# Kernel tuning notes

Measured on AMD Instinct MI355X. Metric: run time of the kernel, lower is better.

Reference implementation:

```python
import jax, jax.numpy as jnp
import numpy as np

B, IB, H, W = 32, 103, 256, 256
P, RB, DIM, DEPTH = 16, 8, 192, 3
KS, KP, TOPK, NC = 24, 24, 2, 9
FFH = 2 * DIM  # max(64, int(dim*2)) = 384
TAU = 0.07 + 1e-08


def ln(x, w, b, eps=1e-5):
    m = x.mean(-1, keepdims=True)
    v = ((x - m) ** 2).mean(-1, keepdims=True)
    return (x - m) / jnp.sqrt(v + eps) * w + b


def setup_inputs() -> dict:
    key = jax.random.key(0)
    keys = iter(jax.random.split(key, 40))
    nrm = lambda shape, s=0.02: jax.random.normal(next(keys), shape, jnp.float32) * s
    return {
        "x": jax.random.normal(next(keys), (B, IB, H, W), jnp.float32),
        "band_w": nrm((RB, IB), 0.05), "band_b": jnp.zeros((RB,), jnp.float32),
        "dw_w": nrm((RB, P, P), 0.05), "pw_w": nrm((DIM, RB), 0.1),
        "pe_ln_w": jnp.ones((DIM,), jnp.float32), "pe_ln_b": jnp.zeros((DIM,), jnp.float32),
        "spec_proto": nrm((KS, RB)), "spat_proto": nrm((KP, DIM)),
        "r1_w": nrm((DIM, 128), 0.05), "r1_b": jnp.zeros((128,), jnp.float32),
        "r2_w": nrm((128, KS + KP), 0.05), "r2_b": jnp.zeros((KS + KP,), jnp.float32),
        "key_w": nrm((RB + DIM, DIM), 0.05),
        "pos_bias": jnp.zeros((1, 1, DIM), jnp.float32),
        "blk_ln_w": jnp.ones((DEPTH, DIM), jnp.float32), "blk_ln_b": jnp.zeros((DEPTH, DIM), jnp.float32),
        "blk_q_w": nrm((DEPTH, DIM, DIM), 0.05), "blk_v_w": nrm((DEPTH, DIM, DIM), 0.05),
        "blk_f1_w": nrm((DEPTH, DIM, FFH), 0.05), "blk_f1_b": jnp.zeros((DEPTH, FFH), jnp.float32),
        "blk_f2_w": nrm((DEPTH, FFH, DIM), 0.05), "blk_f2_b": jnp.zeros((DEPTH, DIM), jnp.float32),
        "blk_g1": jnp.full((DEPTH, DIM), 0.01, jnp.float32), "blk_g2": jnp.full((DEPTH, DIM), 0.01, jnp.float32),
        "fin_ln_w": jnp.ones((DIM,), jnp.float32), "fin_ln_b": jnp.zeros((DIM,), jnp.float32),
        "head_w": nrm((DIM, NC), 0.01), "head_b": jnp.zeros((NC,), jnp.float32),
    }


def _forward(x, band_w, band_b, dw_w, pw_w, pe_ln_w, pe_ln_b, spec_proto, spat_proto,
             r1_w, r1_b, r2_w, r2_b, key_w, pos_bias,
             blk_ln_w, blk_ln_b, blk_q_w, blk_v_w, blk_f1_w, blk_f1_b, blk_f2_w, blk_f2_b,
             blk_g1, blk_g2, fin_ln_w, fin_ln_b, head_w, head_b):
    # 1x1 band reduction conv: (B,103,H,W) -> (B,8,H,W)
    x_red = jnp.einsum('bchw,oc->bohw', x, band_w) + band_b[None, :, None, None]
    Bn, C, Hh, Ww = x_red.shape
    hp, wp = Hh // P, Ww // P
    # depthwise conv, kernel==stride==P -> non-overlapping patches
    patches = x_red.reshape(Bn, C, hp, P, wp, P)
    dw = jnp.einsum('bcipjq,cpq->bcij', patches, dw_w)        # (B,RB,hp,wp)
    pw = jnp.einsum('bcij,dc->bdij', dw, pw_w)                # (B,DIM,hp,wp)
    tok = pw.reshape(Bn, DIM, hp * wp).transpose(0, 2, 1)     # (B,N,DIM)
    tok = ln(tok, pe_ln_w, pe_ln_b)
    # router -> topk -> softmax gate -> gather prototypes -> weighted sum
    h = jax.nn.gelu(tok @ r1_w + r1_b, approximate=False)
    rlogits = h @ r2_w + r2_b                                 # (B,N,KS+KP)
    s_vals, s_idx = jax.lax.top_k(rlogits[..., :KS], TOPK)
    p_vals, p_idx = jax.lax.top_k(rlogits[..., KS:], TOPK)
    w_s = jax.nn.softmax(s_vals / TAU, axis=-1)               # (B,N,TOPK)
    w_p = jax.nn.softmax(p_vals / TAU, axis=-1)
    spec_mixed = (spec_proto[s_idx] * w_s[..., None]).sum(2)  # (B,N,RB)
    spat_mixed = (spat_proto[p_idx] * w_p[..., None]).sum(2)  # (B,N,DIM)
    keys_t = jnp.concatenate([spec_mixed, spat_mixed], -1) @ key_w + pos_bias  # (B,N,DIM)
    # linear-attention blocks
    xb = tok
    for i in range(DEPTH):
        xn = ln(xb, blk_ln_w[i], blk_ln_b[i])
        q = xn @ blk_q_w[i]
        v = xn @ blk_v_w[i]
        q_s = jax.nn.softmax(q, axis=-1)
        KV = jnp.einsum('bnc,bnd->bcd', keys_t, v)            # (B,C,C)
        out = jnp.einsum('bnc,bcd->bnd', q_s, KV)             # (B,N,C)
        xb = xb + out * blk_g1[i]
        xn2 = ln(xb, blk_ln_w[i], blk_ln_b[i])
        ff = jax.nn.gelu(xn2 @ blk_f1_w[i] + blk_f1_b[i], approximate=False) @ blk_f2_w[i] + blk_f2_b[i]
        xb = xb + ff * blk_g2[i]
    feat = ln(xb.mean(1), fin_ln_w, fin_ln_b)                 # (B,DIM)
    return feat @ head_w + head_b                             # (B,NC)


def reference(x, band_w, band_b, dw_w, pw_w, pe_ln_w, pe_ln_b, spec_proto, spat_proto,
              r1_w, r1_b, r2_w, r2_b, key_w, pos_bias,
              blk_ln_w, blk_ln_b, blk_q_w, blk_v_w, blk_f1_w, blk_f1_b, blk_f2_w, blk_f2_b,
              blk_g1, blk_g2, fin_ln_w, fin_ln_b, head_w, head_b):
    return _forward(x, band_w, band_b, dw_w, pw_w, pe_ln_w, pe_ln_b, spec_proto, spat_proto,
                    r1_w, r1_b, r2_w, r2_b, key_w, pos_bias,
                    blk_ln_w, blk_ln_b, blk_q_w, blk_v_w, blk_f1_w, blk_f1_b, blk_f2_w, blk_f2_b,
                    blk_g1, blk_g2, fin_ln_w, fin_ln_b, head_w, head_b)
```

## Files before the change

kernel.cpp:

```cpp
#include <hip/hip_runtime.h>
#include <math.h>


typedef __attribute__((ext_vector_type(8))) short bf16x8;
typedef __attribute__((ext_vector_type(4))) float f32x4;

__device__ __forceinline__ float wsum64(float v) {
#pragma unroll
  for (int o = 32; o > 0; o >>= 1) v += __shfl_xor(v, o, 64);
  return v;
}
__device__ __forceinline__ float sum16(float v) {
#pragma unroll
  for (int o = 8; o > 0; o >>= 1) v += __shfl_xor(v, o, 64);
  return v;
}
__device__ __forceinline__ float max16(float v) {
#pragma unroll
  for (int o = 8; o > 0; o >>= 1) v = fmaxf(v, __shfl_xor(v, o, 64));
  return v;
}
__device__ __forceinline__ float gelu_f(float x) {
  return 0.5f * x * (1.0f + erff(x * 0.7071067811865476f));
}
__device__ __forceinline__ ushort f2bf(float f) {
  union { float f; unsigned u; } v;
  v.f = f;
  unsigned r = v.u + 0x7FFFu + ((v.u >> 16) & 1u);
  return (ushort)(r >> 16);
}

__global__ __launch_bounds__(256) void prep_w(
    const float* __restrict__ qw, const float* __restrict__ vw,
    const float* __restrict__ f1w, const float* __restrict__ f2w,
    const float* __restrict__ r1_w, const float* __restrict__ r2_w,
    const float* __restrict__ key_w, const float* __restrict__ band_w,
    ushort* __restrict__ qwT, ushort* __restrict__ vwT,
    ushort* __restrict__ f1T, ushort* __restrict__ f2T,
    ushort* __restrict__ r1T, ushort* __restrict__ r2T,
    ushort* __restrict__ keyT, float* __restrict__ bandT) {
  const int i = blockIdx.x * 256 + threadIdx.x;
  if (i < 110592) {
    const int d = i / 36864, r = i % 36864;
    const int k = r / 192, c = r % 192;
    qwT[d * 36864 + c * 192 + k] = f2bf(qw[i]);
    vwT[d * 36864 + c * 192 + k] = f2bf(vw[i]);
  }
  if (i < 221184) {
    const int d = i / 73728, r = i % 73728;
    const int k = r / 384, j = r % 384;
    f1T[d * 73728 + j * 192 + k] = f2bf(f1w[i]);
    const int k2 = r / 192, j2 = r % 192;
    f2T[d * 73728 + j2 * 384 + k2] = f2bf(f2w[i]);
  }
  if (i < 24576) {
    const int j = i / 192, k = i % 192;
    r1T[i] = f2bf(r1_w[k * 128 + j]);
  }
  if (i < 6144) {
    const int j = i / 128, k = i % 128;
    r2T[i] = f2bf(r2_w[k * 48 + j]);
  }
  if (i < 43008) {
    const int j = i / 224, k = i % 224;
    keyT[i] = (k < 200) ? f2bf(key_w[k * 192 + j]) : (ushort)0;
  }
  if (i < 824) {
    const int ch = i >> 3, c = i & 7;
    bandT[i] = band_w[c * 103 + ch];
  }
}

__global__ __launch_bounds__(512) void k1_band_dw(
    const float* __restrict__ x, const float* __restrict__ bandT,
    const float* __restrict__ band_b, const float* __restrict__ dw_w,
    float* __restrict__ dw_out) {
  const int blk = blockIdx.x;
  const int b = blk >> 4, ip = blk & 15;
  const int t = threadIdx.x;
  const int col4 = t & 63;
  const int j = col4 >> 2;
  const int qb = (col4 & 3) << 2;
  const int p0 = t >> 6;

  float acc[8][8];
#pragma unroll
  for (int e = 0; e < 8; ++e)
#pragma unroll
    for (int c = 0; c < 8; ++c) acc[e][c] = 0.f;

  const f32x4* xp = (const f32x4*)x + (size_t)b * (103 * 16384) + (size_t)ip * 1024;

  auto body = [&](const f32x4 v0, const f32x4 v1, const int ch) {
    const f32x4 wA = *(const f32x4*)&bandT[ch * 8];
    const f32x4 wB = *(const f32x4*)&bandT[ch * 8 + 4];
    const float bw[8] = {wA.x, wA.y, wA.z, wA.w, wB.x, wB.y, wB.z, wB.w};
#pragma unroll
    for (int c = 0; c < 8; ++c) {
      acc[0][c] = fmaf(v0.x, bw[c], acc[0][c]);
      acc[1][c] = fmaf(v0.y, bw[c], acc[1][c]);
      acc[2][c] = fmaf(v0.z, bw[c], acc[2][c]);
      acc[3][c] = fmaf(v0.w, bw[c], acc[3][c]);
      acc[4][c] = fmaf(v1.x, bw[c], acc[4][c]);
      acc[5][c] = fmaf(v1.y, bw[c], acc[5][c]);
      acc[6][c] = fmaf(v1.z, bw[c], acc[6][c]);
      acc[7][c] = fmaf(v1.w, bw[c], acc[7][c]);
    }
  };

  f32x4 p0v = __builtin_nontemporal_load(&xp[t]);
  f32x4 p1v = __builtin_nontemporal_load(&xp[t + 512]);
  f32x4 q0v = __builtin_nontemporal_load(&xp[t + 16384]);
  f32x4 q1v = __builtin_nontemporal_load(&xp[t + 16896]);
#pragma unroll 1
  for (int ch = 0; ch < 100; ch += 2) {
    const f32x4 r0 = __builtin_nontemporal_load(&xp[t + 2 * 16384]);
    const f32x4 r1 = __builtin_nontemporal_load(&xp[t + 2 * 16384 + 512]);
    const f32x4 s0 = __builtin_nontemporal_load(&xp[t + 3 * 16384]);
    const f32x4 s1 = __builtin_nontemporal_load(&xp[t + 3 * 16384 + 512]);
    body(p0v, p1v, ch);
    body(q0v, q1v, ch + 1);
    p0v = r0; p1v = r1; q0v = s0; q1v = s1;
    xp += 2 * 16384;
  }
  const f32x4 u0 = __builtin_nontemporal_load(&xp[t + 2 * 16384]);
  const f32x4 u1 = __builtin_nontemporal_load(&xp[t + 2 * 16384 + 512]);
  body(p0v, p1v, 100);
  body(q0v, q1v, 101);
  body(u0, u1, 102);

  float dwt[8];
#pragma unroll
  for (int c = 0; c < 8; ++c) dwt[c] = 0.f;
#pragma unroll
  for (int e = 0; e < 8; ++e) {
    const int pp = p0 + ((e >> 2) << 3);
    const int qq = qb + (e & 3);
#pragma unroll
    for (int c = 0; c < 8; ++c)
      dwt[c] = fmaf(dw_w[c * 256 + pp * 16 + qq], acc[e][c] + band_b[c], dwt[c]);
  }
#pragma unroll
  for (int c = 0; c < 8; ++c) {
    dwt[c] += __shfl_xor(dwt[c], 1, 64);
    dwt[c] += __shfl_xor(dwt[c], 2, 64);
  }
  __shared__ float part[8][16][8];
  if ((t & 3) == 0) {
#pragma unroll
    for (int c = 0; c < 8; ++c) part[t >> 6][j][c] = dwt[c];
  }
  __syncthreads();
  if (t < 128) {
    const int jj = t >> 3, c = t & 7;
    float s = 0.f;
#pragma unroll
    for (int w = 0; w < 8; ++w) s += part[w][jj][c];
    dw_out[(((size_t)b * 16 + ip) * 16 + jj) * 8 + c] = s;
  }
}

__global__ __launch_bounds__(256) void k2_mfma(
    const float* __restrict__ dw, const float* __restrict__ pw_w,
    const float* __restrict__ pe_ln_w, const float* __restrict__ pe_ln_b,
    const float* __restrict__ spec_proto, const float* __restrict__ spat_proto,
    const ushort* __restrict__ r1T, const float* __restrict__ r1_b,
    const ushort* __restrict__ r2T, const float* __restrict__ r2_b,
    const ushort* __restrict__ keyT, const float* __restrict__ pos_bias,
    float* __restrict__ xb_out, ushort* __restrict__ keysT) {
  const int t = threadIdx.x;
  const int lane = t & 63, wid = t >> 6;
  const int wm = wid >> 1, wn = wid & 1;
  const int l15 = lane & 15, lg4 = lane >> 4;
  const int tok0 = blockIdx.x * 32;
  const int rl = wm * 16 + 4 * lg4;
  const int b = blockIdx.x >> 3;
  const int n0 = (blockIdx.x & 7) * 32;

  __shared__ float dw8s[32][8];
  __shared__ __align__(16) ushort s_xn[32][200];
  __shared__ __align__(16) ushort s_w[192][40];
  __shared__ __align__(16) ushort s_h[32][200];
  __shared__ __align__(16) ushort s_mix[32][232];
  __shared__ float s_rl[32][48];
  __shared__ float topwS[32][4];
  __shared__ int   topiS[32][4];

  dw8s[t >> 3][t & 7] = dw[((size_t)tok0 + (t >> 3)) * 8 + (t & 7)];
  __syncthreads();

#pragma unroll
  for (int half = 0; half < 2; ++half) {
    const int tt = half * 16 + (t >> 4), lg = t & 15;
    float pre[12], sm = 0.f;
#pragma unroll
    for (int m = 0; m < 12; ++m) {
      const int d = lg + 16 * m;
      const f32x4 pa = *(const f32x4*)&pw_w[d * 8];
      const f32x4 pb = *(const f32x4*)&pw_w[d * 8 + 4];
      float p = pa.x * dw8s[tt][0] + pa.y * dw8s[tt][1] + pa.z * dw8s[tt][2] +
                pa.w * dw8s[tt][3] + pb.x * dw8s[tt][4] + pb.y * dw8s[tt][5] +
                pb.z * dw8s[tt][6] + pb.w * dw8s[tt][7];
      pre[m] = p;
      sm += p;
    }
    sm = sum16(sm);
    const float mean = sm * (1.f / 192.f);
    float vv = 0.f;
#pragma unroll
    for (int m = 0; m < 12; ++m) {
      const float d0 = pre[m] - mean;
      vv = fmaf(d0, d0, vv);
    }
    vv = sum16(vv);
    const float inv = rsqrtf(vv * (1.f / 192.f) + 1e-5f);
#pragma unroll
    for (int m = 0; m < 12; ++m) {
      const int d = lg + 16 * m;
      const float xv = (pre[m] - mean) * inv * pe_ln_w[d] + pe_ln_b[d];
      s_xn[tt][d] = f2bf(xv);
      xb_out[((size_t)tok0 + tt) * 192 + d] = xv;
    }
  }
  __syncthreads();

  {
    f32x4 hacc[4];
#pragma unroll
    for (int f = 0; f < 4; ++f) hacc[f] = (f32x4){0.f, 0.f, 0.f, 0.f};
#pragma unroll 1
    for (int ks = 0; ks < 6; ++ks) {
#pragma unroll
      for (int i = 0; i < 2; ++i) {
        const int lin = t + 256 * i;
        const int row = lin >> 2, c8 = (lin & 3) * 8;
        *(uint4*)&s_w[row][c8] = *(const uint4*)&r1T[row * 192 + ks * 32 + c8];
      }
      __syncthreads();
      const bf16x8 a = *(const bf16x8*)&s_xn[wm * 16 + l15][ks * 32 + 8 * lg4];
#pragma unroll
      for (int f = 0; f < 4; ++f) {
        const bf16x8 bb = *(const bf16x8*)&s_w[wn * 64 + 16 * f + l15][8 * lg4];
        hacc[f] = __builtin_amdgcn_mfma_f32_16x16x32_bf16(a, bb, hacc[f], 0, 0, 0);
      }
      __syncthreads();
    }
#pragma unroll
    for (int f = 0; f < 4; ++f) {
      const int col = wn * 64 + 16 * f + l15;
#pragma unroll
      for (int reg = 0; reg < 4; ++reg)
        s_h[rl + reg][col] = f2bf(gelu_f(hacc[f][reg] + r1_b[col]));
    }
  }
  __syncthreads();

  {
    f32x4 racc[2];
    racc[0] = (f32x4){0.f, 0.f, 0.f, 0.f};
    racc[1] = (f32x4){0.f, 0.f, 0.f, 0.f};
#pragma unroll 1
    for (int ks = 0; ks < 4; ++ks) {
      if (t < 192) {
        const int row = t >> 2, c8 = (t & 3) * 8;
        *(uint4*)&s_w[row][c8] = *(const uint4*)&r2T[row * 128 + ks * 32 + c8];
      }
      __syncthreads();
      const bf16x8 a = *(const bf16x8*)&s_h[wm * 16 + l15][ks * 32 + 8 * lg4];
      if (wn == 0) {
#pragma unroll
        for (int f = 0; f < 2; ++f) {
          const bf16x8 bb = *(const bf16x8*)&s_w[16 * f + l15][8 * lg4];
          racc[f] = __builtin_amdgcn_mfma_f32_16x16x32_bf16(a, bb, racc[f], 0, 0, 0);
        }
      } else {
        const bf16x8 bb = *(const bf16x8*)&s_w[32 + l15][8 * lg4];
        racc[0] = __builtin_amdgcn_mfma_f32_16x16x32_bf16(a, bb, racc[0], 0, 0, 0);
      }
      __syncthreads();
    }
    if (wn == 0) {
#pragma unroll
      for (int f = 0; f < 2; ++f) {
        const int col = 16 * f + l15;
#pragma unroll
        for (int reg = 0; reg < 4; ++reg)
          s_rl[rl + reg][col] = racc[f][reg] + r2_b[col];
      }
    } else {
      const int col = 32 + l15;
#pragma unroll
      for (int reg = 0; reg < 4; ++reg)
        s_rl[rl + reg][col] = racc[0][reg] + r2_b[col];
    }
  }
  __syncthreads();

  if (t < 64) {
    const int tt = t >> 1, half = t & 1;
    const float* base = &s_rl[tt][half * 24];
    float v0 = -1e30f, v1 = -1e30f;
    int i0 = 0, i1 = 0;
    for (int k = 0; k < 24; ++k) {
      const float vv = base[k];
      if (vv > v0) { v1 = v0; i1 = i0; v0 = vv; i0 = k; }
      else if (vv > v1) { v1 = vv; i1 = k; }
    }
    const float tau = (float)(0.07 + 1e-8);
    const float e1 = expf((v1 - v0) / tau);
    const float inv = 1.f / (1.f + e1);
    topwS[tt][half * 2] = inv;
    topwS[tt][half * 2 + 1] = e1 * inv;
    topiS[tt][half * 2] = i0;
    topiS[tt][half * 2 + 1] = i1;
  }
  __syncthreads();

#pragma unroll
  for (int r = 0; r < 28; ++r) {
    const int f = t + 256 * r;
    const int tok = f / 224, c = f % 224;
    float val = 0.f;
    if (c < 8) {
      val = topwS[tok][0] * spec_proto[topiS[tok][0] * 8 + c] +
            topwS[tok][1] * spec_proto[topiS[tok][1] * 8 + c];
    } else if (c < 200) {
      const int cc = c - 8;
      val = topwS[tok][2] * spat_proto[topiS[tok][2] * 192 + cc] +
            topwS[tok][3] * spat_proto[topiS[tok][3] * 192 + cc];
    }
    s_mix[tok][c] = f2bf(val);
  }
  __syncthreads();

  {
    f32x4 kacc[6];
#pragma unroll
    for (int f = 0; f < 6; ++f) kacc[f] = (f32x4){0.f, 0.f, 0.f, 0.f};
#pragma unroll 1
    for (int ks = 0; ks < 7; ++ks) {
#pragma unroll
      for (int i = 0; i < 3; ++i) {
        const int lin = t + 256 * i;
        const int row = lin >> 2, c8 = (lin & 3) * 8;
        *(uint4*)&s_w[row][c8] = *(const uint4*)&keyT[row * 224 + ks * 32 + c8];
      }
      __syncthreads();
      const bf16x8 a = *(const bf16x8*)&s_mix[wm * 16 + l15][ks * 32 + 8 * lg4];
#pragma unroll
      for (int f = 0; f < 6; ++f) {
        const bf16x8 bb = *(const bf16x8*)&s_w[wn * 96 + 16 * f + l15][8 * lg4];
        kacc[f] = __builtin_amdgcn_mfma_f32_16x16x32_bf16(a, bb, kacc[f], 0, 0, 0);
      }
      __syncthreads();
    }
#pragma unroll
    for (int f = 0; f < 6; ++f) {
      const int col = wn * 96 + 16 * f + l15;
#pragma unroll
      for (int reg = 0; reg < 4; ++reg)
        keysT[((size_t)b * 192 + col) * 256 + n0 + rl + reg] =
            f2bf(kacc[f][reg] + pos_bias[col]);
    }
  }
}

__global__ __launch_bounds__(256) void k3a_mfma(
    const float* __restrict__ xb, const float* __restrict__ lnw,
    const float* __restrict__ lnb, const ushort* __restrict__ qwT,
    const ushort* __restrict__ vwT, ushort* __restrict__ qs_bf,
    ushort* __restrict__ vT, int depth) {
  const int t = threadIdx.x;
  const int lane = t & 63, wid = t >> 6;
  const int wm = wid >> 1, wn = wid & 1;
  const int l15 = lane & 15, lg4 = lane >> 4;
  const int tok0 = blockIdx.x * 32;
  const int b = blockIdx.x >> 3;
  const int n0 = (blockIdx.x & 7) * 32;

  __shared__ __align__(16) char smem[12800 + 30720];
  ushort (*s_xn)[200] = (ushort(*)[200])smem;
  ushort (*s_wq)[40] = (ushort(*)[40])(smem + 12800);
  ushort (*s_wv)[40] = (ushort(*)[40])(smem + 12800 + 15360);
  float (*s_q)[196] = (float(*)[196])(smem + 12800);

  const float* lw = lnw + depth * 192;
  const float* lb = lnb + depth * 192;
#pragma unroll
  for (int half = 0; half < 2; ++half) {
    const int tt = half * 16 + (t >> 4);
    const int lg = t & 15;
    const float* xrow = xb + ((size_t)tok0 + tt) * 192;
    float vals[12], sm = 0.f;
#pragma unroll
    for (int m = 0; m < 12; ++m) {
      vals[m] = xrow[lg + 16 * m];
      sm += vals[m];
    }
    sm = sum16(sm);
    const float mean = sm * (1.f / 192.f);
    float vv = 0.f;
#pragma unroll
    for (int m = 0; m < 12; ++m) {
      const float d0 = vals[m] - mean;
      vv = fmaf(d0, d0, vv);
    }
    vv = sum16(vv);
    const float inv = rsqrtf(vv * (1.f / 192.f) + 1e-5f);
#pragma unroll
    for (int m = 0; m < 12; ++m) {
      const int d = lg + 16 * m;
      s_xn[tt][d] = f2bf((vals[m] - mean) * inv * lw[d] + lb[d]);
    }
  }
  __syncthreads();

  f32x4 aq[6], av[6];
#pragma unroll
  for (int f = 0; f < 6; ++f) {
    aq[f] = (f32x4){0.f, 0.f, 0.f, 0.f};
    av[f] = (f32x4){0.f, 0.f, 0.f, 0.f};
  }
  const ushort* qbase = qwT + depth * 36864;
  const ushort* vbase = vwT + depth * 36864;
#pragma unroll 1
  for (int ks = 0; ks < 6; ++ks) {
#pragma unroll
    for (int i = 0; i < 3; ++i) {
      const int idx = t + 256 * i;
      const int row = idx >> 2, c4 = (idx & 3) * 8;
      *(uint4*)&s_wq[row][c4] = *(const uint4*)&qbase[row * 192 + ks * 32 + c4];
      *(uint4*)&s_wv[row][c4] = *(const uint4*)&vbase[row * 192 + ks * 32 + c4];
    }
    __syncthreads();
    const bf16x8 a = *(const bf16x8*)&s_xn[wm * 16 + l15][ks * 32 + 8 * lg4];
#pragma unroll
    for (int f = 0; f < 6; ++f) {
      const bf16x8 bq = *(const bf16x8*)&s_wq[wn * 96 + 16 * f + l15][8 * lg4];
      const bf16x8 bv = *(const bf16x8*)&s_wv[wn * 96 + 16 * f + l15][8 * lg4];
      aq[f] = __builtin_amdgcn_mfma_f32_16x16x32_bf16(a, bq, aq[f], 0, 0, 0);
      av[f] = __builtin_amdgcn_mfma_f32_16x16x32_bf16(a, bv, av[f], 0, 0, 0);
    }
    __syncthreads();
  }

  const int rl = wm * 16 + 4 * lg4;
#pragma unroll
  for (int f = 0; f < 6; ++f) {
    const int col = wn * 96 + 16 * f + l15;
#pragma unroll
    for (int reg = 0; reg < 4; ++reg) {
      vT[((size_t)b * 192 + col) * 256 + n0 + rl + reg] = f2bf(av[f][reg]);
      s_q[rl + reg][col] = aq[f][reg];
    }
  }
  __syncthreads();

#pragma unroll
  for (int half = 0; half < 2; ++half) {
    const int tt = half * 16 + (t >> 4);
    const int lg = t & 15;
    float vals[12], mx = -1e30f;
#pragma unroll
    for (int m = 0; m < 12; ++m) {
      vals[m] = s_q[tt][lg + 16 * m];
      mx = fmaxf(mx, vals[m]);
    }
    mx = max16(mx);
    float s = 0.f;
#pragma unroll
    for (int m = 0; m < 12; ++m) {
      vals[m] = expf(vals[m] - mx);
      s += vals[m];
    }
    s = sum16(s);
    const float inv = 1.f / s;
#pragma unroll
    for (int m = 0; m < 12; ++m)
      qs_bf[((size_t)tok0 + tt) * 192 + lg + 16 * m] = f2bf(vals[m] * inv);
  }
}

__global__ __launch_bounds__(256) void k3b_mfma(
    const ushort* __restrict__ vT, const ushort* __restrict__ keysT,
    ushort* __restrict__ kvT) {
  const int t = threadIdx.x;
  const int lane = t & 63, wid = t >> 6;
  const int wm = wid >> 1, wn = wid & 1;
  const int l15 = lane & 15, lg4 = lane >> 4;
  const int b = blockIdx.x / 6;
  const int d0 = (blockIdx.x % 6) * 32;

  __shared__ __align__(16) ushort s_a[32][264];
  __shared__ __align__(16) ushort s_w[192][40];

  const ushort* vbase = vT + ((size_t)b * 192 + d0) * 256;
#pragma unroll
  for (int i = 0; i < 4; ++i) {
    const int idx = t + 256 * i;
    const int row = idx >> 5, c8 = (idx & 31) * 8;
    *(uint4*)&s_a[row][c8] = *(const uint4*)&vbase[row * 256 + c8];
  }

  f32x4 acc[6];
#pragma unroll
  for (int f = 0; f < 6; ++f) acc[f] = (f32x4){0.f, 0.f, 0.f, 0.f};
  const ushort* kbase = keysT + (size_t)b * 192 * 256;
#pragma unroll 1
  for (int ks = 0; ks < 8; ++ks) {
#pragma unroll
    for (int i = 0; i < 3; ++i) {
      const int idx = t + 256 * i;
      const int row = idx >> 2, c4 = (idx & 3) * 8;
      *(uint4*)&s_w[row][c4] = *(const uint4*)&kbase[row * 256 + ks * 32 + c4];
    }
    __syncthreads();
    const bf16x8 a = *(const bf16x8*)&s_a[wm * 16 + l15][ks * 32 + 8 * lg4];
#pragma unroll
    for (int f = 0; f < 6; ++f) {
      const bf16x8 bb = *(const bf16x8*)&s_w[wn * 96 + 16 * f + l15][8 * lg4];
      acc[f] = __builtin_amdgcn_mfma_f32_16x16x32_bf16(a, bb, acc[f], 0, 0, 0);
    }
    __syncthreads();
  }

  const int rl = wm * 16 + 4 * lg4;
#pragma unroll
  for (int f = 0; f < 6; ++f) {
    const int col = wn * 96 + 16 * f + l15;
#pragma unroll
    for (int reg = 0; reg < 4; ++reg)
      kvT[((size_t)b * 192 + d0 + rl + reg) * 192 + col] = f2bf(acc[f][reg]);
  }
}

__global__ __launch_bounds__(256) void k3c_mfma(
    float* __restrict__ xb, const ushort* __restrict__ qs_bf,
    const ushort* __restrict__ kvT, const float* __restrict__ lnw,
    const float* __restrict__ lnb, const ushort* __restrict__ f1T,
    const ushort* __restrict__ f2T, const float* __restrict__ f1b,
    const float* __restrict__ f2b, const float* __restrict__ g1,
    const float* __restrict__ g2, int depth) {
  const int t = threadIdx.x;
  const int lane = t & 63, wid = t >> 6;
  const int wm = wid >> 1, wn = wid & 1;
  const int l15 = lane & 15, lg4 = lane >> 4;
  const int tok0 = blockIdx.x * 32;
  const int b = blockIdx.x >> 3;

  __shared__ __align__(16) char smem[12800 + 15360 + 12800 + 512];
  ushort (*s_a)[200] = (ushort(*)[200])smem;
  ushort (*s_w)[40] = (ushort(*)[40])(smem + 12800);
  ushort (*s_ff)[200] = (ushort(*)[200])(smem + 12800 + 15360);
  float (*s_red)[4] = (float(*)[4])(smem + 12800 + 15360 + 12800);

#pragma unroll
  for (int i = 0; i < 3; ++i) {
    const int idx = t + 256 * i;
    const int row = idx / 24, c8 = (idx % 24) * 8;
    *(uint4*)&s_a[row][c8] = *(const uint4*)&qs_bf[((size_t)tok0 + row) * 192 + c8];
  }
  __syncthreads();

  f32x4 o1[6];
#pragma unroll
  for (int f = 0; f < 6; ++f) o1[f] = (f32x4){0.f, 0.f, 0.f, 0.f};
  const ushort* kvb = kvT + (size_t)b * 36864;
#pragma unroll 1
  for (int ks = 0; ks < 6; ++ks) {
#pragma unroll
    for (int i = 0; i < 3; ++i) {
      const int idx = t + 256 * i;
      const int row = idx >> 2, c4 = (idx & 3) * 8;
      *(uint4*)&s_w[row][c4] = *(const uint4*)&kvb[row * 192 + ks * 32 + c4];
    }
    __syncthreads();
    const bf16x8 a = *(const bf16x8*)&s_a[wm * 16 + l15][ks * 32 + 8 * lg4];
#pragma unroll
    for (int f = 0; f < 6; ++f) {
      const bf16x8 bb = *(const bf16x8*)&s_w[wn * 96 + 16 * f + l15][8 * lg4];
      o1[f] = __builtin_amdgcn_mfma_f32_16x16x32_bf16(a, bb, o1[f], 0, 0, 0);
    }
    __syncthreads();
  }

  const float* g1p = g1 + depth * 192;
  const float* lw = lnw + depth * 192;
  const float* lb = lnb + depth * 192;
  const int rl = wm * 16 + 4 * lg4;
  float xbn[6][4];
  float psum[4] = {0.f, 0.f, 0.f, 0.f}, psq[4] = {0.f, 0.f, 0.f, 0.f};
#pragma unroll
  for (int f = 0; f < 6; ++f) {
    const int col = wn * 96 + 16 * f + l15;
#pragma unroll
    for (int reg = 0; reg < 4; ++reg) {
      const float xv =
          xb[((size_t)tok0 + rl + reg) * 192 + col] + o1[f][reg] * g1p[col];
      xbn[f][reg] = xv;
      psum[reg] += xv;
      psq[reg] = fmaf(xv, xv, psq[reg]);
    }
  }
#pragma unroll
  for (int reg = 0; reg < 4; ++reg) {
#pragma unroll
    for (int o = 8; o > 0; o >>= 1) {
      psum[reg] += __shfl_xor(psum[reg], o, 64);
      psq[reg] += __shfl_xor(psq[reg], o, 64);
    }
  }
  if (l15 == 0) {
#pragma unroll
    for (int reg = 0; reg < 4; ++reg) {
      s_red[rl + reg][wn] = psum[reg];
      s_red[rl + reg][2 + wn] = psq[reg];
    }
  }
  __syncthreads();
  float mean[4], inv[4];
#pragma unroll
  for (int reg = 0; reg < 4; ++reg) {
    const float s = s_red[rl + reg][0] + s_red[rl + reg][1];
    const float q = s_red[rl + reg][2] + s_red[rl + reg][3];
    mean[reg] = s * (1.f / 192.f);
    const float var = q * (1.f / 192.f) - mean[reg] * mean[reg];
    inv[reg] = rsqrtf(var + 1e-5f);
  }
#pragma unroll
  for (int f = 0; f < 6; ++f) {
    const int col = wn * 96 + 16 * f + l15;
#pragma unroll
    for (int reg = 0; reg < 4; ++reg)
      s_a[rl + reg][col] =
          f2bf((xbn[f][reg] - mean[reg]) * inv[reg] * lw[col] + lb[col]);
  }
  __syncthreads();

  f32x4 o2[6];
#pragma unroll
  for (int f = 0; f < 6; ++f) o2[f] = (f32x4){0.f, 0.f, 0.f, 0.f};
#pragma unroll 1
  for (int h = 0; h < 2; ++h) {
    f32x4 hh[6];
#pragma unroll
    for (int f = 0; f < 6; ++f) hh[f] = (f32x4){0.f, 0.f, 0.f, 0.f};
    const ushort* f1base = f1T + depth * 73728 + h * 36864;
#pragma unroll 1
    for (int ks = 0; ks < 6; ++ks) {
#pragma unroll
      for (int i = 0; i < 3; ++i) {
        const int idx = t + 256 * i;
        const int row = idx >> 2, c4 = (idx & 3) * 8;
        *(uint4*)&s_w[row][c4] = *(const uint4*)&f1base[row * 192 + ks * 32 + c4];
      }
      __syncthreads();
      const bf16x8 a = *(const bf16x8*)&s_a[wm * 16 + l15][ks * 32 + 8 * lg4];
#pragma unroll
      for (int f = 0; f < 6; ++f) {
        const bf16x8 bb = *(const bf16x8*)&s_w[wn * 96 + 16 * f + l15][8 * lg4];
        hh[f] = __builtin_amdgcn_mfma_f32_16x16x32_bf16(a, bb, hh[f], 0, 0, 0);
      }
      __syncthreads();
    }
    const float* b1p = f1b + depth * 384 + h * 192;
#pragma unroll
    for (int f = 0; f < 6; ++f) {
      const int col = wn * 96 + 16 * f + l15;
#pragma unroll
      for (int reg = 0; reg < 4; ++reg)
        s_ff[rl + reg][col] = f2bf(gelu_f(hh[f][reg] + b1p[col]));
    }
    __syncthreads();
    const ushort* f2base = f2T + depth * 73728;
#pragma unroll 1
    for (int ks2 = 0; ks2 < 6; ++ks2) {
#pragma unroll
      for (int i = 0; i < 3; ++i) {
        const int idx = t + 256 * i;
        const int row = idx >> 2, c4 = (idx & 3) * 8;
        *(uint4*)&s_w[row][c4] =
            *(const uint4*)&f2base[row * 384 + h * 192 + ks2 * 32 + c4];
      }
      __syncthreads();
      const bf16x8 a = *(const bf16x8*)&s_ff[wm * 16 + l15][ks2 * 32 + 8 * lg4];
#pragma unroll
      for (int f = 0; f < 6; ++f) {
        const bf16x8 bb = *(const bf16x8*)&s_w[wn * 96 + 16 * f + l15][8 * lg4];
        o2[f] = __builtin_amdgcn_mfma_f32_16x16x32_bf16(a, bb, o2[f], 0, 0, 0);
      }
      __syncthreads();
    }
  }

  const float* b2p = f2b + depth * 192;
  const float* g2p = g2 + depth * 192;
#pragma unroll
  for (int f = 0; f < 6; ++f) {
    const int col = wn * 96 + 16 * f + l15;
#pragma unroll
    for (int reg = 0; reg < 4; ++reg)
      xb[((size_t)tok0 + rl + reg) * 192 + col] =
          xbn[f][reg] + (o2[f][reg] + b2p[col]) * g2p[col];
  }
}

__global__ __launch_bounds__(192) void k4_head(
    const float* __restrict__ xb, const float* __restrict__ flnw,
    const float* __restrict__ flnb, const float* __restrict__ hw,
    const float* __restrict__ hb, float* __restrict__ out) {
  const int b = blockIdx.x, t = threadIdx.x;
  const int w = t >> 6, lane = t & 63;
  float s = 0.f;
  const float* base = xb + (size_t)b * 256 * 192 + t;
#pragma unroll 4
  for (int n = 0; n < 256; ++n) s += base[n * 192];
  const float feat_pre = s * (1.f / 256.f);
  __shared__ float red[3];
  __shared__ float feat[192];
  float sm = wsum64(feat_pre);
  if (lane == 0) red[w] = sm;
  __syncthreads();
  const float mean = (red[0] + red[1] + red[2]) * (1.f / 192.f);
  __syncthreads();
  const float dd = feat_pre - mean;
  sm = wsum64(dd * dd);
  if (lane == 0) red[w] = sm;
  __syncthreads();
  const float var = (red[0] + red[1] + red[2]) * (1.f / 192.f);
  feat[t] = dd * rsqrtf(var + 1e-5f) * flnw[t] + flnb[t];
  __syncthreads();
  if (t < 9) {
    float a = hb[t];
    for (int d = 0; d < 192; ++d) a = fmaf(feat[d], hw[d * 9 + t], a);
    out[b * 9 + t] = a;
  }
}

extern "C" void kernel_launch(void* const* d_in, const int* in_sizes, int n_in,
                              void* d_out, int out_size, void* d_ws, size_t ws_size,
                              hipStream_t stream) {
  (void)in_sizes; (void)n_in; (void)out_size; (void)ws_size;
  const float* x          = (const float*)d_in[0];
  const float* band_w     = (const float*)d_in[1];
  const float* band_b     = (const float*)d_in[2];
  const float* dw_w       = (const float*)d_in[3];
  const float* pw_w       = (const float*)d_in[4];
  const float* pe_ln_w    = (const float*)d_in[5];
  const float* pe_ln_b    = (const float*)d_in[6];
  const float* spec_proto = (const float*)d_in[7];
  const float* spat_proto = (const float*)d_in[8];
  const float* r1_w       = (const float*)d_in[9];
  const float* r1_b       = (const float*)d_in[10];
  const float* r2_w       = (const float*)d_in[11];
  const float* r2_b       = (const float*)d_in[12];
  const float* key_w      = (const float*)d_in[13];
  const float* pos_bias   = (const float*)d_in[14];
  const float* blk_ln_w   = (const float*)d_in[15];
  const float* blk_ln_b   = (const float*)d_in[16];
  const float* blk_q_w    = (const float*)d_in[17];
  const float* blk_v_w    = (const float*)d_in[18];
  const float* blk_f1_w   = (const float*)d_in[19];
  const float* blk_f1_b   = (const float*)d_in[20];
  const float* blk_f2_w   = (const float*)d_in[21];
  const float* blk_f2_b   = (const float*)d_in[22];
  const float* blk_g1     = (const float*)d_in[23];
  const float* blk_g2     = (const float*)d_in[24];
  const float* fin_ln_w   = (const float*)d_in[25];
  const float* fin_ln_b   = (const float*)d_in[26];
  const float* head_w     = (const float*)d_in[27];
  const float* head_b     = (const float*)d_in[28];

  float* ws    = (float*)d_ws;
  float* dw    = ws;
  float* xbuf  = dw + 65536;
  float* bandT = xbuf + 1572864;
  ushort* ush    = (ushort*)(bandT + 1024);
  ushort* qs_bf  = ush;
  ushort* kvT    = qs_bf + 1572864;
  ushort* keysT  = kvT + 1179648;
  ushort* vT     = keysT + 1572864;
  ushort* qwT    = vT + 1572864;
  ushort* vwT    = qwT + 110592;
  ushort* f1T    = vwT + 110592;
  ushort* f2T    = f1T + 221184;
  ushort* r1T    = f2T + 221184;
  ushort* r2T    = r1T + 24576;
  ushort* keyT   = r2T + 6144;

  prep_w<<<864, 256, 0, stream>>>(blk_q_w, blk_v_w, blk_f1_w, blk_f2_w,
                                  r1_w, r2_w, key_w, band_w,
                                  qwT, vwT, f1T, f2T, r1T, r2T, keyT, bandT);
  k1_band_dw<<<512, 512, 0, stream>>>(x, bandT, band_b, dw_w, dw);
  k2_mfma<<<256, 256, 0, stream>>>(dw, pw_w, pe_ln_w, pe_ln_b, spec_proto,
                                   spat_proto, r1T, r1_b, r2T, r2_b, keyT,
                                   pos_bias, xbuf, keysT);
  for (int d = 0; d < 3; ++d) {
    k3a_mfma<<<256, 256, 0, stream>>>(xbuf, blk_ln_w, blk_ln_b, qwT, vwT,
                                      qs_bf, vT, d);
    k3b_mfma<<<192, 256, 0, stream>>>(vT, keysT, kvT);
    k3c_mfma<<<256, 256, 0, stream>>>(xbuf, qs_bf, kvT, blk_ln_w, blk_ln_b,
                                      f1T, f2T, blk_f1_b, blk_f2_b, blk_g1,
                                      blk_g2, d);
  }
  k4_head<<<32, 192, 0, stream>>>(xbuf, fin_ln_w, fin_ln_b, head_w, head_b,
                                  (float*)d_out);
}
```

Baseline: 333.2 us.

## Split band-reduction kernel into 2048 smaller blocks with deeper channel prefetch

The band-reduction plus depthwise kernel now gives each block a quarter of a patch row-group: 256 threads each handling one float4 per channel, launched as 2048 blocks instead of 512 blocks of 512 threads. Each thread holds half as many accumulators and prefetches four channels ahead instead of two. The final reduction now uses wider shuffles and a smaller shared buffer. The aim is more blocks, higher occupancy and more loads in flight on this memory-bound read of the ~860MB input. The cost is more blocks and a more scattered per-block access pattern of 256-byte row segments.

```diff
diff --git a/kernel.cpp b/kernel.cpp
--- a/kernel.cpp
+++ b/kernel.cpp
@@ -71,92 +71,94 @@
   }
 }
 
-__global__ __launch_bounds__(512) void k1_band_dw(
+__global__ __launch_bounds__(256) void k1_band_dw(
     const float* __restrict__ x, const float* __restrict__ bandT,
     const float* __restrict__ band_b, const float* __restrict__ dw_w,
     float* __restrict__ dw_out) {
   const int blk = blockIdx.x;
-  const int b = blk >> 4, ip = blk & 15;
+  const int cq = blk & 3;
+  const int ip = (blk >> 2) & 15;
+  const int b = blk >> 6;
   const int t = threadIdx.x;
-  const int col4 = t & 63;
-  const int j = col4 >> 2;
-  const int qb = (col4 & 3) << 2;
-  const int p0 = t >> 6;
-
-  float acc[8][8];
-#pragma unroll
-  for (int e = 0; e < 8; ++e)
+  const int row = t >> 4;
+  const int c16 = t & 15;
+
+  float acc[4][8];
+#pragma unroll
+  for (int e = 0; e < 4; ++e)
 #pragma unroll
     for (int c = 0; c < 8; ++c) acc[e][c] = 0.f;
 
-  const f32x4* xp = (const f32x4*)x + (size_t)b * (103 * 16384) + (size_t)ip * 1024;
-
-  auto body = [&](const f32x4 v0, const f32x4 v1, const int ch) {
+  const f32x4* xp = (const f32x4*)(x + (size_t)b * (103 * 65536) +
+                                   (size_t)ip * 4096 + cq * 64) +
+                    row * 64 + c16;
+  const int CS = 16384;
+
+  auto body = [&](const f32x4 v, const int ch) {
     const f32x4 wA = *(const f32x4*)&bandT[ch * 8];
     const f32x4 wB = *(const f32x4*)&bandT[ch * 8 + 4];
     const float bw[8] = {wA.x, wA.y, wA.z, wA.w, wB.x, wB.y, wB.z, wB.w};
 #pragma unroll
     for (int c = 0; c < 8; ++c) {
-      acc[0][c] = fmaf(v0.x, bw[c], acc[0][c]);
-      acc[1][c] = fmaf(v0.y, bw[c], acc[1][c]);
-      acc[2][c] = fmaf(v0.z, bw[c], acc[2][c]);
-      acc[3][c] = fmaf(v0.w, bw[c], acc[3][c]);
-      acc[4][c] = fmaf(v1.x, bw[c], acc[4][c]);
-      acc[5][c] = fmaf(v1.y, bw[c], acc[5][c]);
-      acc[6][c] = fmaf(v1.z, bw[c], acc[6][c]);
-      acc[7][c] = fmaf(v1.w, bw[c], acc[7][c]);
+      acc[0][c] = fmaf(v.x, bw[c], acc[0][c]);
+      acc[1][c] = fmaf(v.y, bw[c], acc[1][c]);
+      acc[2][c] = fmaf(v.z, bw[c], acc[2][c]);
+      acc[3][c] = fmaf(v.w, bw[c], acc[3][c]);
     }
   };
 
-  f32x4 p0v = __builtin_nontemporal_load(&xp[t]);
-  f32x4 p1v = __builtin_nontemporal_load(&xp[t + 512]);
-  f32x4 q0v = __builtin_nontemporal_load(&xp[t + 16384]);
-  f32x4 q1v = __builtin_nontemporal_load(&xp[t + 16896]);
-#pragma unroll 1
-  for (int ch = 0; ch < 100; ch += 2) {
-    const f32x4 r0 = __builtin_nontemporal_load(&xp[t + 2 * 16384]);
-    const f32x4 r1 = __builtin_nontemporal_load(&xp[t + 2 * 16384 + 512]);
-    const f32x4 s0 = __builtin_nontemporal_load(&xp[t + 3 * 16384]);
-    const f32x4 s1 = __builtin_nontemporal_load(&xp[t + 3 * 16384 + 512]);
-    body(p0v, p1v, ch);
-    body(q0v, q1v, ch + 1);
-    p0v = r0; p1v = r1; q0v = s0; q1v = s1;
-    xp += 2 * 16384;
-  }
-  const f32x4 u0 = __builtin_nontemporal_load(&xp[t + 2 * 16384]);
-  const f32x4 u1 = __builtin_nontemporal_load(&xp[t + 2 * 16384 + 512]);
-  body(p0v, p1v, 100);
-  body(q0v, q1v, 101);
-  body(u0, u1, 102);
-
+  f32x4 v0 = __builtin_nontemporal_load(xp + 0 * CS);
+  f32x4 v1 = __builtin_nontemporal_load(xp + 1 * CS);
+  f32x4 v2 = __builtin_nontemporal_load(xp + 2 * CS);
+  f32x4 v3 = __builtin_nontemporal_load(xp + 3 * CS);
+#pragma unroll 1
+  for (int ch = 0; ch < 100; ch += 4) {
+    const int p1 = min(ch + 5, 102), p2 = min(ch + 6, 102), p3 = min(ch + 7, 102);
+    const f32x4 n0 = __builtin_nontemporal_load(xp + (ch + 4) * CS);
+    const f32x4 n1 = __builtin_nontemporal_load(xp + p1 * CS);
+    const f32x4 n2 = __builtin_nontemporal_load(xp + p2 * CS);
+    const f32x4 n3 = __builtin_nontemporal_load(xp + p3 * CS);
+    body(v0, ch);
+    body(v1, ch + 1);
+    body(v2, ch + 2);
+    body(v3, ch + 3);
+    v0 = n0; v1 = n1; v2 = n2; v3 = n3;
+  }
+  body(v0, 100);
+  body(v1, 101);
+  body(v2, 102);
+
+  const int q0 = (c16 & 3) << 2;
   float dwt[8];
 #pragma unroll
   for (int c = 0; c < 8; ++c) dwt[c] = 0.f;
 #pragma unroll
-  for (int e = 0; e < 8; ++e) {
-    const int pp = p0 + ((e >> 2) << 3);
-    const int qq = qb + (e & 3);
+  for (int e = 0; e < 4; ++e) {
 #pragma unroll
     for (int c = 0; c < 8; ++c)
-      dwt[c] = fmaf(dw_w[c * 256 + pp * 16 + qq], acc[e][c] + band_b[c], dwt[c]);
+      dwt[c] = fmaf(dw_w[c * 256 + row * 16 + q0 + e], acc[e][c] + band_b[c],
+                    dwt[c]);
   }
 #pragma unroll
   for (int c = 0; c < 8; ++c) {
     dwt[c] += __shfl_xor(dwt[c], 1, 64);
     dwt[c] += __shfl_xor(dwt[c], 2, 64);
-  }
-  __shared__ float part[8][16][8];
-  if ((t & 3) == 0) {
-#pragma unroll
-    for (int c = 0; c < 8; ++c) part[t >> 6][j][c] = dwt[c];
-  }
-  __syncthreads();
-  if (t < 128) {
+    dwt[c] += __shfl_xor(dwt[c], 16, 64);
+    dwt[c] += __shfl_xor(dwt[c], 32, 64);
+  }
+  __shared__ float part[4][4][8];
+  const int w = t >> 6, lane = t & 63;
+  if ((lane & 51) == 0) {
+    const int jl = (lane >> 2) & 3;
+#pragma unroll
+    for (int c = 0; c < 8; ++c) part[w][jl][c] = dwt[c];
+  }
+  __syncthreads();
+  if (t < 32) {
     const int jj = t >> 3, c = t & 7;
-    float s = 0.f;
-#pragma unroll
-    for (int w = 0; w < 8; ++w) s += part[w][jj][c];
-    dw_out[(((size_t)b * 16 + ip) * 16 + jj) * 8 + c] = s;
+    const float s =
+        part[0][jj][c] + part[1][jj][c] + part[2][jj][c] + part[3][jj][c];
+    dw_out[(((size_t)b * 16 + ip) * 16 + cq * 4 + jj) * 8 + c] = s;
   }
 }
 
@@ -791,7 +793,7 @@
   prep_w<<<864, 256, 0, stream>>>(blk_q_w, blk_v_w, blk_f1_w, blk_f2_w,
                                   r1_w, r2_w, key_w, band_w,
                                   qwT, vwT, f1T, f2T, r1T, r2T, keyT, bandT);
-  k1_band_dw<<<512, 512, 0, stream>>>(x, bandT, band_b, dw_w, dw);
+  k1_band_dw<<<2048, 256, 0, stream>>>(x, bandT, band_b, dw_w, dw);
   k2_mfma<<<256, 256, 0, stream>>>(dw, pw_w, pe_ln_w, pe_ln_b, spec_proto,
                                    spat_proto, r1T, r1_b, r2T, r2_b, keyT,
                                    pos_bias, xbuf, keysT);
```

New measurement: 345.7 us. 1.04x slower.

## Prefetch weight tiles into registers and double-buffer LDS in MFMA GEMM loops

Applied to the files above, without the earlier changes.

The weight-tile loops in the QV projection, KV, and block-MLP kernels now issue the global loads for the next K-slice into registers before running the current slice's MFMAs, then write them to shared memory afterwards. k3b and k3c use two LDS buffers, so each step needs one barrier instead of two. In k3c the prefetch also carries across GEMM stages (KV into FF1, FF1 into FF2, and so on), which hides the first-tile latency of each stage. The cost is more registers and more shared memory, which may reduce occupancy.

```diff
diff --git a/kernel.cpp b/kernel.cpp
--- a/kernel.cpp
+++ b/kernel.cpp
@@ -413,6 +413,16 @@
       s_xn[tt][d] = f2bf((vals[m] - mean) * inv * lw[d] + lb[d]);
     }
   }
+
+  const ushort* qbase = qwT + depth * 36864;
+  const ushort* vbase = vwT + depth * 36864;
+#pragma unroll
+  for (int i = 0; i < 3; ++i) {
+    const int idx = t + 256 * i;
+    const int row = idx >> 2, c4 = (idx & 3) * 8;
+    *(uint4*)&s_wq[row][c4] = *(const uint4*)&qbase[row * 192 + c4];
+    *(uint4*)&s_wv[row][c4] = *(const uint4*)&vbase[row * 192 + c4];
+  }
   __syncthreads();
 
   f32x4 aq[6], av[6];
@@ -421,18 +431,18 @@
     aq[f] = (f32x4){0.f, 0.f, 0.f, 0.f};
     av[f] = (f32x4){0.f, 0.f, 0.f, 0.f};
   }
-  const ushort* qbase = qwT + depth * 36864;
-  const ushort* vbase = vwT + depth * 36864;
+  uint4 preq[3], prev_[3];
 #pragma unroll 1
   for (int ks = 0; ks < 6; ++ks) {
-#pragma unroll
-    for (int i = 0; i < 3; ++i) {
-      const int idx = t + 256 * i;
-      const int row = idx >> 2, c4 = (idx & 3) * 8;
-      *(uint4*)&s_wq[row][c4] = *(const uint4*)&qbase[row * 192 + ks * 32 + c4];
-      *(uint4*)&s_wv[row][c4] = *(const uint4*)&vbase[row * 192 + ks * 32 + c4];
-    }
-    __syncthreads();
+    if (ks < 5) {
+#pragma unroll
+      for (int i = 0; i < 3; ++i) {
+        const int idx = t + 256 * i;
+        const int row = idx >> 2, c4 = (idx & 3) * 8;
+        preq[i] = *(const uint4*)&qbase[row * 192 + (ks + 1) * 32 + c4];
+        prev_[i] = *(const uint4*)&vbase[row * 192 + (ks + 1) * 32 + c4];
+      }
+    }
     const bf16x8 a = *(const bf16x8*)&s_xn[wm * 16 + l15][ks * 32 + 8 * lg4];
 #pragma unroll
     for (int f = 0; f < 6; ++f) {
@@ -442,6 +452,16 @@
       av[f] = __builtin_amdgcn_mfma_f32_16x16x32_bf16(a, bv, av[f], 0, 0, 0);
     }
     __syncthreads();
+    if (ks < 5) {
+#pragma unroll
+      for (int i = 0; i < 3; ++i) {
+        const int idx = t + 256 * i;
+        const int row = idx >> 2, c4 = (idx & 3) * 8;
+        *(uint4*)&s_wq[row][c4] = preq[i];
+        *(uint4*)&s_wv[row][c4] = prev_[i];
+      }
+      __syncthreads();
+    }
   }
 
   const int rl = wm * 16 + 4 * lg4;
@@ -492,8 +512,18 @@
   const int d0 = (blockIdx.x % 6) * 32;
 
   __shared__ __align__(16) ushort s_a[32][264];
-  __shared__ __align__(16) ushort s_w[192][40];
-
+  __shared__ __align__(16) ushort s_w[2][192][40];
+
+  const ushort* kbase = keysT + (size_t)b * 192 * 256;
+  uint4 pre[3];
+  int cur = 0;
+
+#pragma unroll
+  for (int i = 0; i < 3; ++i) {
+    const int idx = t + 256 * i;
+    const int row = idx >> 2, c4 = (idx & 3) * 8;
+    pre[i] = *(const uint4*)&kbase[row * 256 + c4];
+  }
   const ushort* vbase = vT + ((size_t)b * 192 + d0) * 256;
 #pragma unroll
   for (int i = 0; i < 4; ++i) {
@@ -501,27 +531,43 @@
     const int row = idx >> 5, c8 = (idx & 31) * 8;
     *(uint4*)&s_a[row][c8] = *(const uint4*)&vbase[row * 256 + c8];
   }
+#pragma unroll
+  for (int i = 0; i < 3; ++i) {
+    const int idx = t + 256 * i;
+    const int row = idx >> 2, c4 = (idx & 3) * 8;
+    *(uint4*)&s_w[0][row][c4] = pre[i];
+  }
+  __syncthreads();
 
   f32x4 acc[6];
 #pragma unroll
   for (int f = 0; f < 6; ++f) acc[f] = (f32x4){0.f, 0.f, 0.f, 0.f};
-  const ushort* kbase = keysT + (size_t)b * 192 * 256;
 #pragma unroll 1
   for (int ks = 0; ks < 8; ++ks) {
-#pragma unroll
-    for (int i = 0; i < 3; ++i) {
-      const int idx = t + 256 * i;
-      const int row = idx >> 2, c4 = (idx & 3) * 8;
-      *(uint4*)&s_w[row][c4] = *(const uint4*)&kbase[row * 256 + ks * 32 + c4];
+    if (ks < 7) {
+#pragma unroll
+      for (int i = 0; i < 3; ++i) {
+        const int idx = t + 256 * i;
+        const int row = idx >> 2, c4 = (idx & 3) * 8;
+        pre[i] = *(const uint4*)&kbase[row * 256 + (ks + 1) * 32 + c4];
+      }
+    }
+    const bf16x8 a = *(const bf16x8*)&s_a[wm * 16 + l15][ks * 32 + 8 * lg4];
+#pragma unroll
+    for (int f = 0; f < 6; ++f) {
+      const bf16x8 bb = *(const bf16x8*)&s_w[cur][wn * 96 + 16 * f + l15][8 * lg4];
+      acc[f] = __builtin_amdgcn_mfma_f32_16x16x32_bf16(a, bb, acc[f], 0, 0, 0);
+    }
+    if (ks < 7) {
+#pragma unroll
+      for (int i = 0; i < 3; ++i) {
+        const int idx = t + 256 * i;
+        const int row = idx >> 2, c4 = (idx & 3) * 8;
+        *(uint4*)&s_w[cur ^ 1][row][c4] = pre[i];
+      }
     }
     __syncthreads();
-    const bf16x8 a = *(const bf16x8*)&s_a[wm * 16 + l15][ks * 32 + 8 * lg4];
-#pragma unroll
-    for (int f = 0; f < 6; ++f) {
-      const bf16x8 bb = *(const bf16x8*)&s_w[wn * 96 + 16 * f + l15][8 * lg4];
-      acc[f] = __builtin_amdgcn_mfma_f32_16x16x32_bf16(a, bb, acc[f], 0, 0, 0);
-    }
-    __syncthreads();
+    cur ^= 1;
   }
 
   const int rl = wm * 16 + 4 * lg4;
@@ -548,41 +594,69 @@
   const int tok0 = blockIdx.x * 32;
   const int b = blockIdx.x >> 3;
 
-  __shared__ __align__(16) char smem[12800 + 15360 + 12800 + 512];
-  ushort (*s_a)[200] = (ushort(*)[200])smem;
-  ushort (*s_w)[40] = (ushort(*)[40])(smem + 12800);
-  ushort (*s_ff)[200] = (ushort(*)[200])(smem + 12800 + 15360);
-  float (*s_red)[4] = (float(*)[4])(smem + 12800 + 15360 + 12800);
-
+  __shared__ __align__(16) ushort s_a[32][200];
+  __shared__ __align__(16) ushort s_w[2][192][40];
+  __shared__ __align__(16) ushort s_ff[32][200];
+  __shared__ float s_red[32][4];
+
+  uint4 pre[3];
+  int cur = 0;
+  auto LOADW = [&](const ushort* base, int stride, int ks) {
+#pragma unroll
+    for (int i = 0; i < 3; ++i) {
+      const int idx = t + 256 * i;
+      const int row = idx >> 2, c4 = (idx & 3) * 8;
+      pre[i] = *(const uint4*)&base[row * stride + ks * 32 + c4];
+    }
+  };
+  auto WRITEW = [&](int buf) {
+#pragma unroll
+    for (int i = 0; i < 3; ++i) {
+      const int idx = t + 256 * i;
+      const int row = idx >> 2, c4 = (idx & 3) * 8;
+      *(uint4*)&s_w[buf][row][c4] = pre[i];
+    }
+  };
+  auto run6 = [&](f32x4* acc, const ushort (*Asrc)[200], const ushort* base,
+                  int stride, const ushort* nxt, int nstride) {
+#pragma unroll 1
+    for (int ks = 0; ks < 6; ++ks) {
+      const bool lastk = (ks == 5);
+      const bool hn = !lastk || (nxt != nullptr);
+      if (hn) LOADW(lastk ? nxt : base, lastk ? nstride : stride,
+                    lastk ? 0 : ks + 1);
+      const bf16x8 a = *(const bf16x8*)&Asrc[wm * 16 + l15][ks * 32 + 8 * lg4];
+#pragma unroll
+      for (int f = 0; f < 6; ++f) {
+        const bf16x8 bb =
+            *(const bf16x8*)&s_w[cur][wn * 96 + 16 * f + l15][8 * lg4];
+        acc[f] = __builtin_amdgcn_mfma_f32_16x16x32_bf16(a, bb, acc[f], 0, 0, 0);
+      }
+      if (hn) WRITEW(cur ^ 1);
+      __syncthreads();
+      cur ^= 1;
+    }
+  };
+
+  const ushort* kvb = kvT + (size_t)b * 36864;
+  const ushort* f1b0 = f1T + depth * 73728;
+  const ushort* f1b1 = f1b0 + 36864;
+  const ushort* f2bb = f2T + depth * 73728;
+
+  LOADW(kvb, 192, 0);
 #pragma unroll
   for (int i = 0; i < 3; ++i) {
     const int idx = t + 256 * i;
     const int row = idx / 24, c8 = (idx % 24) * 8;
     *(uint4*)&s_a[row][c8] = *(const uint4*)&qs_bf[((size_t)tok0 + row) * 192 + c8];
   }
+  WRITEW(0);
   __syncthreads();
 
   f32x4 o1[6];
 #pragma unroll
   for (int f = 0; f < 6; ++f) o1[f] = (f32x4){0.f, 0.f, 0.f, 0.f};
-  const ushort* kvb = kvT + (size_t)b * 36864;
-#pragma unroll 1
-  for (int ks = 0; ks < 6; ++ks) {
-#pragma unroll
-    for (int i = 0; i < 3; ++i) {
-      const int idx = t + 256 * i;
-      const int row = idx >> 2, c4 = (idx & 3) * 8;
-      *(uint4*)&s_w[row][c4] = *(const uint4*)&kvb[row * 192 + ks * 32 + c4];
-    }
-    __syncthreads();
-    const bf16x8 a = *(const bf16x8*)&s_a[wm * 16 + l15][ks * 32 + 8 * lg4];
-#pragma unroll
-    for (int f = 0; f < 6; ++f) {
-      const bf16x8 bb = *(const bf16x8*)&s_w[wn * 96 + 16 * f + l15][8 * lg4];
-      o1[f] = __builtin_amdgcn_mfma_f32_16x16x32_bf16(a, bb, o1[f], 0, 0, 0);
-    }
-    __syncthreads();
-  }
+  run6(o1, s_a, kvb, 192, f1b0, 192);
 
   const float* g1p = g1 + depth * 192;
   const float* lw = lnw + depth * 192;
@@ -640,30 +714,13 @@
   f32x4 o2[6];
 #pragma unroll
   for (int f = 0; f < 6; ++f) o2[f] = (f32x4){0.f, 0.f, 0.f, 0.f};
-#pragma unroll 1
-  for (int h = 0; h < 2; ++h) {
+
+  {
     f32x4 hh[6];
 #pragma unroll
     for (int f = 0; f < 6; ++f) hh[f] = (f32x4){0.f, 0.f, 0.f, 0.f};
-    const ushort* f1base = f1T + depth * 73728 + h * 36864;
-#pragma unroll 1
-    for (int ks = 0; ks < 6; ++ks) {
-#pragma unroll
-      for (int i = 0; i < 3; ++i) {
-        const int idx = t + 256 * i;
-        const int row = idx >> 2, c4 = (idx & 3) * 8;
-        *(uint4*)&s_w[row][c4] = *(const uint4*)&f1base[row * 192 + ks * 32 + c4];
-      }
-      __syncthreads();
-      const bf16x8 a = *(const bf16x8*)&s_a[wm * 16 + l15][ks * 32 + 8 * lg4];
-#pragma unroll
-      for (int f = 0; f < 6; ++f) {
-        const bf16x8 bb = *(const bf16x8*)&s_w[wn * 96 + 16 * f + l15][8 * lg4];
-        hh[f] = __builtin_amdgcn_mfma_f32_16x16x32_bf16(a, bb, hh[f], 0, 0, 0);
-      }
-      __syncthreads();
-    }
-    const float* b1p = f1b + depth * 384 + h * 192;
+    run6(hh, s_a, f1b0, 192, f2bb, 384);
+    const float* b1p = f1b + depth * 384;
 #pragma unroll
     for (int f = 0; f < 6; ++f) {
       const int col = wn * 96 + 16 * f + l15;
@@ -672,25 +729,23 @@
         s_ff[rl + reg][col] = f2bf(gelu_f(hh[f][reg] + b1p[col]));
     }
     __syncthreads();
-    const ushort* f2base = f2T + depth * 73728;
-#pragma unroll 1
-    for (int ks2 = 0; ks2 < 6; ++ks2) {
-#pragma unroll
-      for (int i = 0; i < 3; ++i) {
-        const int idx = t + 256 * i;
-        const int row = idx >> 2, c4 = (idx & 3) * 8;
-        *(uint4*)&s_w[row][c4] =
-            *(const uint4*)&f2base[row * 384 + h * 192 + ks2 * 32 + c4];
-      }
-      __syncthreads();
-      const bf16x8 a = *(const bf16x8*)&s_ff[wm * 16 + l15][ks2 * 32 + 8 * lg4];
-#pragma unroll
-      for (int f = 0; f < 6; ++f) {
-        const bf16x8 bb = *(const bf16x8*)&s_w[wn * 96 + 16 * f + l15][8 * lg4];
-        o2[f] = __builtin_amdgcn_mfma_f32_16x16x32_bf16(a, bb, o2[f], 0, 0, 0);
-      }
-      __syncthreads();
-    }
+    run6(o2, s_ff, f2bb, 384, f1b1, 192);
+  }
+  {
+    f32x4 hh[6];
+#pragma unroll
+    for (int f = 0; f < 6; ++f) hh[f] = (f32x4){0.f, 0.f, 0.f, 0.f};
+    run6(hh, s_a, f1b1, 192, f2bb + 192, 384);
+    const float* b1p = f1b + depth * 384 + 192;
+#pragma unroll
+    for (int f = 0; f < 6; ++f) {
+      const int col = wn * 96 + 16 * f + l15;
+#pragma unroll
+      for (int reg = 0; reg < 4; ++reg)
+        s_ff[rl + reg][col] = f2bf(gelu_f(hh[f][reg] + b1p[col]));
+    }
+    __syncthreads();
+    run6(o2, s_ff, f2bb + 192, 384, nullptr, 0);
   }
 
   const float* b2p = f2b + depth * 192;
```

After: 400.4 us. 1.2x slower.
